# Kernel optimization log

Hardware: AMD Instinct MI355X
Metric: run time of the kernel (lower is better)

Reference implementation:

```python
import jax, jax.numpy as jnp
import numpy as np

HIDDEN = 512
FEAT = 128   # input features to GRU (inputs last dim = FEAT + 1 shock column)
BATCH = 128
SEQ = 512
DENSE1 = 64
BN_EPS = 1e-3  # Keras BatchNormalization default epsilon


def setup_inputs() -> dict:
    key = jax.random.key(0)
    ks = jax.random.split(key, 12)
    s = 0.05
    inputs = jax.random.normal(ks[0], (BATCH, SEQ, FEAT + 1), dtype=jnp.float32)
    return {
        "inputs": inputs,
        # GRU params (Keras reset_after=True layout: gates ordered z, r, h)
        "kernel": jax.random.normal(ks[1], (FEAT, 3 * HIDDEN), jnp.float32) * s,
        "recurrent_kernel": jax.random.normal(ks[2], (HIDDEN, 3 * HIDDEN), jnp.float32) * s,
        "bias": jax.random.normal(ks[3], (2, 3 * HIDDEN), jnp.float32) * s,  # [input_bias, recurrent_bias]
        # head
        "W1": jax.random.normal(ks[4], (HIDDEN, DENSE1), jnp.float32) * s,
        "b1": jnp.zeros((DENSE1,), jnp.float32),
        "gamma": jnp.ones((DENSE1,), jnp.float32),
        "beta": jnp.zeros((DENSE1,), jnp.float32),
        "moving_mean": jnp.zeros((DENSE1,), jnp.float32),
        "moving_var": jnp.ones((DENSE1,), jnp.float32),
        "W2": jax.random.normal(ks[5], (DENSE1, 1), jnp.float32) * s,
        "b2": jnp.zeros((1,), jnp.float32),
        "W_shock": jax.random.normal(ks[6], (1,), jnp.float32),
    }


def _gru_scan(x, h0, kernel, recurrent_kernel, bias):
    # x: [B,T,F] -> scan over time. Keras GRU v2 (reset_after=True):
    #   z = sig(x Wz + bzi + h Uz + bzr); r = sig(x Wr + ...);
    #   hh = tanh(x Wh + bhi + r*(h Uh + bhr)); h = z*h + (1-z)*hh
    b_i, b_r = bias[0], bias[1]
    xt = jnp.transpose(x, (1, 0, 2))  # [T,B,F]
    # precompute input projections for all steps: [T,B,3H]
    x_proj = jnp.einsum("tbf,fh->tbh", xt, kernel) + b_i
    H = h0.shape[-1]

    def step(h, xp):
        hp = h @ recurrent_kernel + b_r  # [B,3H]
        xz, xr, xh = xp[:, :H], xp[:, H:2 * H], xp[:, 2 * H:]
        hz, hr, hh_ = hp[:, :H], hp[:, H:2 * H], hp[:, 2 * H:]
        z = jax.nn.sigmoid(xz + hz)
        r = jax.nn.sigmoid(xr + hr)
        hh = jnp.tanh(xh + r * hh_)
        h_new = z * h + (1.0 - z) * hh
        return h_new, h_new

    state, seq = jax.lax.scan(step, h0, x_proj)
    return jnp.transpose(seq, (1, 0, 2)), state  # gru_out [B,T,H], state [B,H]


def reference(inputs, kernel, recurrent_kernel, bias, W1, b1, gamma, beta,
              moving_mean, moving_var, W2, b2, W_shock):
    x = inputs[:, :, :-1]            # [B,T,F]
    shock = inputs[:, :, -1]         # [B,T]
    h0 = jnp.zeros((x.shape[0], HIDDEN), x.dtype)
    gru_out, state = _gru_scan(x, h0, kernel, recurrent_kernel, bias)
    # shock effect: tile shock to [B,T,H], * W_shock, mean over time -> [B,H]
    shock_mean = jnp.mean(shock, axis=1, keepdims=True)  # [B,1]
    state = state + shock_mean * W_shock  # broadcasts to [B,H]
    # head (inference mode: dropout is identity, BN uses moving stats)
    h = jax.nn.relu(state @ W1 + b1)
    h = (h - moving_mean) * jax.lax.rsqrt(moving_var + BN_EPS) * gamma + beta
    return h @ W2 + b2  # [B,1]
```

## Files before the change

kernel.cpp:

```cpp
#include <hip/hip_runtime.h>
#include <hip/hip_fp16.h>

typedef _Float16 f16;
typedef _Float16 f16x8 __attribute__((ext_vector_type(8)));
typedef float    f32x4 __attribute__((ext_vector_type(4)));

#define HID 512
#define FEA 128
#define ROWSTR 129
#define SEQL 512
#define DEN1 64
#define NG 8
#define WPG 32
#define MB 16
#define GC 16
#define THREADS 256
#define KTOT 640

#define WS_CTR    0
#define WS_FLG    256
#define WS_HRING  4096
#define WS_SM     (WS_HRING + 262144)
#define WS_HPART  (WS_SM + 1024)
#define WS_END    (WS_HPART + 16384)

#define AT_LD(p)  __hip_atomic_load((p),  __ATOMIC_RELAXED, __HIP_MEMORY_SCOPE_AGENT)

union H4 { unsigned long long u; f16 h[4]; };

__device__ __forceinline__ f16x8 ld_h16(const f16* p) {
    f16x8 r;
    asm volatile("global_load_dwordx4 %0, %1, off sc0 sc1" : "=v"(r) : "v"(p));
    return r;
}
__device__ __forceinline__ void st_h64(void* p, unsigned long long v) {
    asm volatile("global_store_dwordx2 %0, %1, off sc0 sc1" :: "v"(p), "v"(v) : "memory");
}
__device__ __forceinline__ unsigned ld_flag(const unsigned* p) {
    unsigned r;
    asm volatile("global_load_dword %0, %1, off sc0 sc1" : "=v"(r) : "v"(p) : "memory");
    asm volatile("s_waitcnt vmcnt(0)" ::: "memory");
    return r;
}
__device__ __forceinline__ void st_flag(unsigned* p, unsigned v) {
    asm volatile("global_store_dword %0, %1, off sc0 sc1" :: "v"(p), "v"(v) : "memory");
}
__device__ __forceinline__ void wait_vm0() {
    asm volatile("s_waitcnt vmcnt(0)" ::: "memory");
    __builtin_amdgcn_sched_barrier(0);
}

__device__ __forceinline__ float sigmoid_f(float x) {
    x = fminf(fmaxf(x, -30.f), 30.f);
    return 1.f / (1.f + __expf(-x));
}
__device__ __forceinline__ float tanh_f(float x) {
    x = fminf(fmaxf(x, -15.f), 15.f);
    float e = __expf(2.f * x);
    return (e - 1.f) / (e + 1.f);
}

__global__ __launch_bounds__(THREADS)
void gru_fused(const float* __restrict__ inp, const float* __restrict__ Wk,
               const float* __restrict__ Rk,  const float* __restrict__ bias,
               const float* __restrict__ W1,  const float* __restrict__ b1,
               const float* __restrict__ gam, const float* __restrict__ bet,
               const float* __restrict__ mmn, const float* __restrict__ mvr,
               const float* __restrict__ W2,  const float* __restrict__ b2p,
               const float* __restrict__ Wsh, float* __restrict__ out,
               char* __restrict__ ws)
{
    __shared__ __align__(16) f16 Bl[KTOT * 48];
    __shared__ float red[4096];
    __shared__ __align__(8) f16 htile[256];

    const int tid  = threadIdx.x;
    const int g    = blockIdx.x & (NG - 1);
    const int wgk  = blockIdx.x >> 3;
    const int lane = tid & 63;
    const int wave = tid >> 6;
    const int j0   = wgk * GC;

    unsigned* ctr   = (unsigned*)(ws + WS_CTR);
    unsigned* flg   = (unsigned*)(ws + WS_FLG);
    f16*      hring = (f16*)(ws + WS_HRING);
    float*    smw   = (float*)(ws + WS_SM);
    float*    hpart = (float*)(ws + WS_HPART);

    for (int idx = tid; idx < KTOT * 48; idx += THREADS) {
        int kk  = idx / 48;
        int c   = idx - kk * 48;
        int col = (c >> 4) * HID + j0 + (c & 15);
        float v = (kk < HID) ? Rk[(size_t)kk * 1536 + col]
                             : Wk[(size_t)(kk - HID) * 1536 + col];
        Bl[((size_t)(kk >> 3) * 48 + c) * 8 + (kk & 7)] = (f16)v;
    }

    if (wgk < MB) {
        int b = g * MB + wgk;
        float a = 0.f;
        for (int t = tid; t < SEQL; t += THREADS)
            a += inp[((size_t)b * SEQL + t) * ROWSTR + FEA];
        red[tid] = a;
        __syncthreads();
        for (int s = THREADS / 2; s > 0; s >>= 1) {
            if (tid < s) red[tid] += red[tid + s];
            __syncthreads();
        }
        if (tid == 0) smw[b] = red[0] * (1.f / SEQL);
    }

    const int brow = tid >> 4;
    const int jcol = j0 + (tid & 15);
    const float bZ  = bias[jcol]           + bias[1536 + jcol];
    const float bR  = bias[512 + jcol]     + bias[1536 + 512 + jcol];
    const float bXH = bias[1024 + jcol];
    const float bHH = bias[1536 + 1024 + jcol];

    const int arow  = lane & 15;
    const int ahalf = lane >> 4;

    float xa[4][8];
    if (wave == 3) {
        const float* xb = inp + ((size_t)(g * MB + arow) * SEQL + 0) * ROWSTR + ahalf * 8;
        #pragma unroll
        for (int s = 0; s < 4; ++s)
            #pragma unroll
            for (int q = 0; q < 8; ++q)
                xa[s][q] = xb[s * 32 + q];
    }

    float hold = 0.f;
    __syncthreads();

    for (int t = 0; t < SEQL; ++t) {
        const int cur = t & 1;
        const f16* hb = hring + ((size_t)cur * NG + g) * MB * HID
                              + (size_t)arow * HID + ahalf * 8;

        f32x4 aZ = {0,0,0,0}, aR = {0,0,0,0}, aH = {0,0,0,0}, aX = {0,0,0,0};

        if (wave < 3) {
            f16x8 af[5];
            #pragma unroll
            for (int s = 0; s < 5; ++s)
                af[s] = ld_h16(hb + (wave * 5 + s) * 32);
            wait_vm0();
            #pragma unroll
            for (int s = 0; s < 5; ++s) {
                int ks = wave * 5 + s;
                const f16x8* bp = ((const f16x8*)Bl) + (ks * 4 + ahalf) * 48 + (lane & 15);
                f16x8 bz = bp[0], br = bp[16], bh = bp[32];
                aZ = __builtin_amdgcn_mfma_f32_16x16x32_f16(af[s], bz, aZ, 0, 0, 0);
                aR = __builtin_amdgcn_mfma_f32_16x16x32_f16(af[s], br, aR, 0, 0, 0);
                aH = __builtin_amdgcn_mfma_f32_16x16x32_f16(af[s], bh, aH, 0, 0, 0);
            }
        } else {
            f16x8 af0 = ld_h16(hb + 15 * 32);
            f16x8 afx[4];
            #pragma unroll
            for (int s = 0; s < 4; ++s) {
                f16x8 a;
                #pragma unroll
                for (int q = 0; q < 8; ++q) a[q] = (f16)xa[s][q];
                afx[s] = a;
            }
            wait_vm0();
            {
                const f16x8* bp = ((const f16x8*)Bl) + (15 * 4 + ahalf) * 48 + (lane & 15);
                aZ = __builtin_amdgcn_mfma_f32_16x16x32_f16(af0, bp[0],  aZ, 0, 0, 0);
                aR = __builtin_amdgcn_mfma_f32_16x16x32_f16(af0, bp[16], aR, 0, 0, 0);
                aH = __builtin_amdgcn_mfma_f32_16x16x32_f16(af0, bp[32], aH, 0, 0, 0);
            }
            #pragma unroll
            for (int s = 0; s < 4; ++s) {
                int ks = 16 + s;
                const f16x8* bp = ((const f16x8*)Bl) + (ks * 4 + ahalf) * 48 + (lane & 15);
                aZ = __builtin_amdgcn_mfma_f32_16x16x32_f16(afx[s], bp[0],  aZ, 0, 0, 0);
                aR = __builtin_amdgcn_mfma_f32_16x16x32_f16(afx[s], bp[16], aR, 0, 0, 0);
                aX = __builtin_amdgcn_mfma_f32_16x16x32_f16(afx[s], bp[32], aX, 0, 0, 0);
            }
        }

        #pragma unroll
        for (int i = 0; i < 4; ++i) {
            int ridx = (ahalf * 4 + i) * 16 + (lane & 15);
            red[wave * 1024 +       ridx] = aZ[i];
            red[wave * 1024 + 256 + ridx] = aR[i];
            red[wave * 1024 + 512 + ridx] = aH[i];
        }
        if (wave == 3) {
            #pragma unroll
            for (int i = 0; i < 4; ++i) {
                int ridx = (ahalf * 4 + i) * 16 + (lane & 15);
                red[3 * 1024 + 768 + ridx] = aX[i];
            }
            {
                int tt = (t + 1 < SEQL) ? t + 1 : SEQL - 1;
                const float* xb = inp + ((size_t)(g * MB + arow) * SEQL + tt) * ROWSTR + ahalf * 8;
                #pragma unroll
                for (int s = 0; s < 4; ++s)
                    #pragma unroll
                    for (int q = 0; q < 8; ++q)
                        xa[s][q] = xb[s * 32 + q];
            }
        }
        __syncthreads();

        float zp = red[tid] + red[1024 + tid] + red[2048 + tid] + red[3072 + tid];
        float rp = red[256 + tid] + red[1280 + tid] + red[2304 + tid] + red[3328 + tid];
        float hp = red[512 + tid] + red[1536 + tid] + red[2560 + tid] + red[3584 + tid];
        float xp = red[3840 + tid];

        float z = sigmoid_f(zp + bZ);
        float r = sigmoid_f(rp + bR);
        float hcand = tanh_f((xp + bXH) + r * (hp + bHH));
        float hnew = z * hold + (1.f - z) * hcand;
        f16 h16 = (f16)hnew;
        hold = (float)h16;
        htile[brow * 16 + (tid & 15)] = h16;
        __syncthreads();

        if (tid < 64) {
            int row = tid >> 2, q = tid & 3;
            unsigned long long val = *(const unsigned long long*)(htile + row * 16 + q * 4);
            st_h64(hring + (((size_t)(cur ^ 1) * NG + g) * MB + row) * HID + j0 + q * 4, val);
        }
        if (wave == 0) {
            asm volatile("s_waitcnt vmcnt(0)" ::: "memory");
            if (lane == 0) st_flag(flg + g * 32 + wgk, (unsigned)(t + 1));
            const unsigned want = (unsigned)(t + 1);
            for (;;) {
                unsigned v = ld_flag(flg + g * 32 + (lane & 31));
                if (__all((int)(v >= want))) break;
            }
        }
        __syncthreads();
    }

    const unsigned long long* hfq = (const unsigned long long*)
        (hring + ((size_t)g * MB + brow) * HID);
    const int sub = tid & 15;
    const int c0 = wgk * 2;
    float p0 = 0.f, p1 = 0.f, w0 = 0.f, w1 = 0.f;
    for (int c8 = 0; c8 < 8; ++c8) {
        H4 x; x.u = AT_LD(hfq + sub * 8 + c8);
        #pragma unroll
        for (int e = 0; e < 4; ++e) {
            int k = sub * 32 + c8 * 4 + e;
            float hv = (float)x.h[e];
            float a0 = W1[(size_t)k * DEN1 + c0];
            float a1 = W1[(size_t)k * DEN1 + c0 + 1];
            p0 += hv * a0; p1 += hv * a1; w0 += a0; w1 += a1;
        }
    }
    red[tid] = p0; red[256 + tid] = w0; red[512 + tid] = p1; red[768 + tid] = w1;
    __syncthreads();
    if (tid < 32) {
        int b = tid >> 1, cc = tid & 1;
        int c = c0 + cc;
        float dot = 0.f, wsum = 0.f;
        for (int i = 0; i < 16; ++i) {
            dot  += red[cc * 512 + b * 16 + i];
            wsum += red[cc * 512 + 256 + b * 16 + i];
        }
        float sW = smw[g * MB + b] * Wsh[0];
        float d = dot + sW * wsum + b1[c];
        d = fmaxf(d, 0.f);
        d = (d - mmn[c]) * rsqrtf(mvr[c] + 0.001f) * gam[c] + bet[c];
        red[1024 + tid] = d * W2[c];
    }
    __syncthreads();
    if (tid < MB)
        hpart[((size_t)g * WPG + wgk) * MB + tid] = red[1024 + tid * 2] + red[1024 + tid * 2 + 1];
    __syncthreads();
    if (tid == 0) {
        __builtin_amdgcn_fence(__ATOMIC_RELEASE, "agent");
        unsigned* c9 = ctr + g;
        unsigned old = __hip_atomic_fetch_add(c9, 1u, __ATOMIC_RELAXED, __HIP_MEMORY_SCOPE_AGENT);
        if (old != WPG - 1)
            while (__hip_atomic_load(c9, __ATOMIC_RELAXED, __HIP_MEMORY_SCOPE_AGENT) < WPG) {}
        __builtin_amdgcn_fence(__ATOMIC_ACQUIRE, "agent");
    }
    __syncthreads();
    if (wgk == 0 && tid < MB) {
        float o = b2p[0];
        for (int k = 0; k < WPG; ++k)
            o += hpart[((size_t)g * WPG + k) * MB + tid];
        out[g * MB + tid] = o;
    }
}

extern "C" void kernel_launch(void* const* d_in, const int* in_sizes, int n_in,
                              void* d_out, int out_size, void* d_ws, size_t ws_size,
                              hipStream_t stream) {
    (void)in_sizes; (void)n_in; (void)out_size; (void)ws_size;
    const float* inp  = (const float*)d_in[0];
    const float* Wk   = (const float*)d_in[1];
    const float* Rk   = (const float*)d_in[2];
    const float* bias = (const float*)d_in[3];
    const float* W1   = (const float*)d_in[4];
    const float* b1   = (const float*)d_in[5];
    const float* gam  = (const float*)d_in[6];
    const float* bet  = (const float*)d_in[7];
    const float* mmn  = (const float*)d_in[8];
    const float* mvr  = (const float*)d_in[9];
    const float* W2   = (const float*)d_in[10];
    const float* b2p  = (const float*)d_in[11];
    const float* Wsh  = (const float*)d_in[12];

    hipMemsetAsync(d_ws, 0, WS_END, stream);
    hipLaunchKernelGGL(gru_fused, dim3(NG * WPG), dim3(THREADS), 0, stream,
                       inp, Wk, Rk, bias, W1, b1, gam, bet, mmn, mvr, W2, b2p, Wsh,
                       (float*)d_out, (char*)d_ws);
}
```

Baseline: 1.386 ms.

## Split work by gate across waves and overlap input projection with flag wait

Each of waves 0-2 now computes one gate's full K=512 recurrent product instead of splitting K across four waves, which removes the cross-wave partial-sum reduction. Wave 3 computes the input projection for the next step, biases folded in and double-buffered in shared memory, while wave 0 spins on the inter-block flag barrier, taking it off the critical path. The h tile is written with per-thread 16-bit stores instead of an LDS staging pass, and custom barriers use only the needed waitcnt. The cost is 16 outstanding global loads per wave and many small stores, with a one-step-ahead x pipeline that must stay correctly synchronised.

```diff
diff --git a/kernel.cpp b/kernel.cpp
--- a/kernel.cpp
+++ b/kernel.cpp
@@ -15,7 +15,8 @@
 #define MB 16
 #define GC 16
 #define THREADS 256
-#define KTOT 640
+#define KH 512
+#define KX 128
 
 #define WS_CTR    0
 #define WS_FLG    256
@@ -24,30 +25,41 @@
 #define WS_HPART  (WS_SM + 1024)
 #define WS_END    (WS_HPART + 16384)
 
-#define AT_LD(p)  __hip_atomic_load((p),  __ATOMIC_RELAXED, __HIP_MEMORY_SCOPE_AGENT)
-
-union H4 { unsigned long long u; f16 h[4]; };
-
-__device__ __forceinline__ f16x8 ld_h16(const f16* p) {
-    f16x8 r;
-    asm volatile("global_load_dwordx4 %0, %1, off sc0 sc1" : "=v"(r) : "v"(p));
+__device__ __forceinline__ void st_h2(void* p, unsigned v) {
+    asm volatile("global_store_short %0, %1, off sc0 sc1" :: "v"(p), "v"(v) : "memory");
+}
+__device__ __forceinline__ unsigned long long ld_u64c(const void* p) {
+    unsigned long long r;
+    asm volatile("global_load_dwordx2 %0, %1, off sc0 sc1" : "=v"(r) : "v"(p));
+    asm volatile("s_waitcnt vmcnt(0)" ::: "memory");
     return r;
 }
-__device__ __forceinline__ void st_h64(void* p, unsigned long long v) {
-    asm volatile("global_store_dwordx2 %0, %1, off sc0 sc1" :: "v"(p), "v"(v) : "memory");
-}
-__device__ __forceinline__ unsigned ld_flag(const unsigned* p) {
+__device__ __forceinline__ unsigned ld_flag32(const unsigned* p) {
     unsigned r;
     asm volatile("global_load_dword %0, %1, off sc0 sc1" : "=v"(r) : "v"(p) : "memory");
     asm volatile("s_waitcnt vmcnt(0)" ::: "memory");
     return r;
 }
-__device__ __forceinline__ void st_flag(unsigned* p, unsigned v) {
+__device__ __forceinline__ void st_flag32(unsigned* p, unsigned v) {
     asm volatile("global_store_dword %0, %1, off sc0 sc1" :: "v"(p), "v"(v) : "memory");
 }
 __device__ __forceinline__ void wait_vm0() {
     asm volatile("s_waitcnt vmcnt(0)" ::: "memory");
     __builtin_amdgcn_sched_barrier(0);
+}
+__device__ __forceinline__ void barrier_lgkm() {
+    asm volatile("s_waitcnt lgkmcnt(0)" ::: "memory");
+    __builtin_amdgcn_sched_barrier(0);
+    __builtin_amdgcn_s_barrier();
+    __builtin_amdgcn_sched_barrier(0);
+    asm volatile("" ::: "memory");
+}
+__device__ __forceinline__ void barrier_vm0() {
+    asm volatile("s_waitcnt vmcnt(0) lgkmcnt(0)" ::: "memory");
+    __builtin_amdgcn_sched_barrier(0);
+    __builtin_amdgcn_s_barrier();
+    __builtin_amdgcn_sched_barrier(0);
+    asm volatile("" ::: "memory");
 }
 
 __device__ __forceinline__ float sigmoid_f(float x) {
@@ -70,9 +82,9 @@
                const float* __restrict__ Wsh, float* __restrict__ out,
                char* __restrict__ ws)
 {
-    __shared__ __align__(16) f16 Bl[KTOT * 48];
-    __shared__ float red[4096];
-    __shared__ __align__(8) f16 htile[256];
+    __shared__ __align__(16) f16 Bh[KH * 48];
+    __shared__ __align__(16) f16 Bx[KX * 48];
+    __shared__ float red[2304];
 
     const int tid  = threadIdx.x;
     const int g    = blockIdx.x & (NG - 1);
@@ -87,13 +99,15 @@
     float*    smw   = (float*)(ws + WS_SM);
     float*    hpart = (float*)(ws + WS_HPART);
 
-    for (int idx = tid; idx < KTOT * 48; idx += THREADS) {
-        int kk  = idx / 48;
-        int c   = idx - kk * 48;
+    for (int idx = tid; idx < KH * 48; idx += THREADS) {
+        int kk = idx / 48, c = idx - kk * 48;
         int col = (c >> 4) * HID + j0 + (c & 15);
-        float v = (kk < HID) ? Rk[(size_t)kk * 1536 + col]
-                             : Wk[(size_t)(kk - HID) * 1536 + col];
-        Bl[((size_t)(kk >> 3) * 48 + c) * 8 + (kk & 7)] = (f16)v;
+        Bh[((kk >> 3) * 48 + c) * 8 + (kk & 7)] = (f16)Rk[(size_t)kk * 1536 + col];
+    }
+    for (int idx = tid; idx < KX * 48; idx += THREADS) {
+        int kk = idx / 48, c = idx - kk * 48;
+        int col = (c >> 4) * HID + j0 + (c & 15);
+        Bx[((kk >> 3) * 48 + c) * 8 + (kk & 7)] = (f16)Wk[(size_t)kk * 1536 + col];
     }
 
     if (wgk < MB) {
@@ -112,139 +126,130 @@
 
     const int brow = tid >> 4;
     const int jcol = j0 + (tid & 15);
-    const float bZ  = bias[jcol]           + bias[1536 + jcol];
-    const float bR  = bias[512 + jcol]     + bias[1536 + 512 + jcol];
-    const float bXH = bias[1024 + jcol];
-    const float bHH = bias[1536 + 1024 + jcol];
-
     const int arow  = lane & 15;
     const int ahalf = lane >> 4;
+    const int lcol  = j0 + (lane & 15);
+    const float bZ3  = bias[lcol] + bias[1536 + lcol];
+    const float bR3  = bias[512 + lcol] + bias[1536 + 512 + lcol];
+    const float bX3  = bias[1024 + lcol];
+    const float bHH3 = bias[1536 + 1024 + lcol];
 
     float xa[4][8];
+
+    auto x_window = [&](int t) {
+        f16x8 afx[4];
+        #pragma unroll
+        for (int s = 0; s < 4; ++s) {
+            f16x8 a;
+            #pragma unroll
+            for (int q = 0; q < 8; ++q) a[q] = (f16)xa[s][q];
+            afx[s] = a;
+        }
+        f32x4 az = {0,0,0,0}, ar = {0,0,0,0}, ah = {0,0,0,0};
+        #pragma unroll
+        for (int s = 0; s < 4; ++s) {
+            const f16x8* bx = ((const f16x8*)Bx) + (s * 4 + ahalf) * 48 + (lane & 15);
+            az = __builtin_amdgcn_mfma_f32_16x16x32_f16(afx[s], bx[0],  az, 0, 0, 0);
+            ar = __builtin_amdgcn_mfma_f32_16x16x32_f16(afx[s], bx[16], ar, 0, 0, 0);
+            ah = __builtin_amdgcn_mfma_f32_16x16x32_f16(afx[s], bx[32], ah, 0, 0, 0);
+        }
+        float* xo = red + 768 + ((t + 1) & 1) * 768;
+        #pragma unroll
+        for (int i = 0; i < 4; ++i) {
+            int rix = (ahalf * 4 + i) * 16 + (lane & 15);
+            xo[rix]       = az[i] + bZ3;
+            xo[256 + rix] = ar[i] + bR3;
+            xo[512 + rix] = ah[i] + bX3;
+        }
+        int tt = (t + 2 < SEQL) ? t + 2 : SEQL - 1;
+        const float* xs = inp + ((size_t)(g * MB + arow) * SEQL + tt) * ROWSTR + ahalf * 8;
+        #pragma unroll
+        for (int s = 0; s < 4; ++s)
+            #pragma unroll
+            for (int q = 0; q < 8; ++q)
+                xa[s][q] = xs[s * 32 + q];
+    };
+
+    __syncthreads();
+
     if (wave == 3) {
-        const float* xb = inp + ((size_t)(g * MB + arow) * SEQL + 0) * ROWSTR + ahalf * 8;
+        const float* xs = inp + ((size_t)(g * MB + arow) * SEQL + 0) * ROWSTR + ahalf * 8;
         #pragma unroll
         for (int s = 0; s < 4; ++s)
             #pragma unroll
             for (int q = 0; q < 8; ++q)
-                xa[s][q] = xb[s * 32 + q];
+                xa[s][q] = xs[s * 32 + q];
+        x_window(-1);
     }
 
     float hold = 0.f;
-    __syncthreads();
 
     for (int t = 0; t < SEQL; ++t) {
         const int cur = t & 1;
-        const f16* hb = hring + ((size_t)cur * NG + g) * MB * HID
-                              + (size_t)arow * HID + ahalf * 8;
-
-        f32x4 aZ = {0,0,0,0}, aR = {0,0,0,0}, aH = {0,0,0,0}, aX = {0,0,0,0};
 
         if (wave < 3) {
-            f16x8 af[5];
-            #pragma unroll
-            for (int s = 0; s < 5; ++s)
-                af[s] = ld_h16(hb + (wave * 5 + s) * 32);
+            const f16* hb = hring + ((size_t)cur * NG + g) * MB * HID
+                                  + (size_t)arow * HID + ahalf * 8;
+            f16x8 af[16];
+            #pragma unroll
+            for (int s = 0; s < 16; ++s)
+                asm volatile("global_load_dwordx4 %0, %1, off offset:%c2 sc0 sc1"
+                             : "=v"(af[s]) : "v"(hb), "i"(s * 64));
             wait_vm0();
-            #pragma unroll
-            for (int s = 0; s < 5; ++s) {
-                int ks = wave * 5 + s;
-                const f16x8* bp = ((const f16x8*)Bl) + (ks * 4 + ahalf) * 48 + (lane & 15);
-                f16x8 bz = bp[0], br = bp[16], bh = bp[32];
-                aZ = __builtin_amdgcn_mfma_f32_16x16x32_f16(af[s], bz, aZ, 0, 0, 0);
-                aR = __builtin_amdgcn_mfma_f32_16x16x32_f16(af[s], br, aR, 0, 0, 0);
-                aH = __builtin_amdgcn_mfma_f32_16x16x32_f16(af[s], bh, aH, 0, 0, 0);
+            f32x4 a0 = {0,0,0,0}, a1 = {0,0,0,0};
+            const f16x8* bp = ((const f16x8*)Bh) + ahalf * 48 + wave * GC + (lane & 15);
+            #pragma unroll
+            for (int s = 0; s < 16; s += 2) {
+                a0 = __builtin_amdgcn_mfma_f32_16x16x32_f16(af[s],     bp[s * 192],       a0, 0, 0, 0);
+                a1 = __builtin_amdgcn_mfma_f32_16x16x32_f16(af[s + 1], bp[(s + 1) * 192], a1, 0, 0, 0);
             }
-        } else {
-            f16x8 af0 = ld_h16(hb + 15 * 32);
-            f16x8 afx[4];
-            #pragma unroll
-            for (int s = 0; s < 4; ++s) {
-                f16x8 a;
-                #pragma unroll
-                for (int q = 0; q < 8; ++q) a[q] = (f16)xa[s][q];
-                afx[s] = a;
-            }
-            wait_vm0();
-            {
-                const f16x8* bp = ((const f16x8*)Bl) + (15 * 4 + ahalf) * 48 + (lane & 15);
-                aZ = __builtin_amdgcn_mfma_f32_16x16x32_f16(af0, bp[0],  aZ, 0, 0, 0);
-                aR = __builtin_amdgcn_mfma_f32_16x16x32_f16(af0, bp[16], aR, 0, 0, 0);
-                aH = __builtin_amdgcn_mfma_f32_16x16x32_f16(af0, bp[32], aH, 0, 0, 0);
-            }
-            #pragma unroll
-            for (int s = 0; s < 4; ++s) {
-                int ks = 16 + s;
-                const f16x8* bp = ((const f16x8*)Bl) + (ks * 4 + ahalf) * 48 + (lane & 15);
-                aZ = __builtin_amdgcn_mfma_f32_16x16x32_f16(afx[s], bp[0],  aZ, 0, 0, 0);
-                aR = __builtin_amdgcn_mfma_f32_16x16x32_f16(afx[s], bp[16], aR, 0, 0, 0);
-                aX = __builtin_amdgcn_mfma_f32_16x16x32_f16(afx[s], bp[32], aX, 0, 0, 0);
-            }
-        }
-
-        #pragma unroll
-        for (int i = 0; i < 4; ++i) {
-            int ridx = (ahalf * 4 + i) * 16 + (lane & 15);
-            red[wave * 1024 +       ridx] = aZ[i];
-            red[wave * 1024 + 256 + ridx] = aR[i];
-            red[wave * 1024 + 512 + ridx] = aH[i];
-        }
-        if (wave == 3) {
-            #pragma unroll
-            for (int i = 0; i < 4; ++i) {
-                int ridx = (ahalf * 4 + i) * 16 + (lane & 15);
-                red[3 * 1024 + 768 + ridx] = aX[i];
-            }
-            {
-                int tt = (t + 1 < SEQL) ? t + 1 : SEQL - 1;
-                const float* xb = inp + ((size_t)(g * MB + arow) * SEQL + tt) * ROWSTR + ahalf * 8;
-                #pragma unroll
-                for (int s = 0; s < 4; ++s)
-                    #pragma unroll
-                    for (int q = 0; q < 8; ++q)
-                        xa[s][q] = xb[s * 32 + q];
-            }
-        }
-        __syncthreads();
-
-        float zp = red[tid] + red[1024 + tid] + red[2048 + tid] + red[3072 + tid];
-        float rp = red[256 + tid] + red[1280 + tid] + red[2304 + tid] + red[3328 + tid];
-        float hp = red[512 + tid] + red[1536 + tid] + red[2560 + tid] + red[3584 + tid];
-        float xp = red[3840 + tid];
-
-        float z = sigmoid_f(zp + bZ);
-        float r = sigmoid_f(rp + bR);
-        float hcand = tanh_f((xp + bXH) + r * (hp + bHH));
-        float hnew = z * hold + (1.f - z) * hcand;
-        f16 h16 = (f16)hnew;
-        hold = (float)h16;
-        htile[brow * 16 + (tid & 15)] = h16;
-        __syncthreads();
-
-        if (tid < 64) {
-            int row = tid >> 2, q = tid & 3;
-            unsigned long long val = *(const unsigned long long*)(htile + row * 16 + q * 4);
-            st_h64(hring + (((size_t)(cur ^ 1) * NG + g) * MB + row) * HID + j0 + q * 4, val);
-        }
+            f32x4 acc = a0 + a1;
+            float badd = (wave == 2) ? bHH3 : 0.f;
+            #pragma unroll
+            for (int i = 0; i < 4; ++i)
+                red[wave * 256 + (ahalf * 4 + i) * 16 + (lane & 15)] = acc[i] + badd;
+        }
+        barrier_lgkm();
+
+        {
+            float hzs = red[tid];
+            float hrs = red[256 + tid];
+            float hhs = red[512 + tid];
+            const float* xi = red + 768 + (t & 1) * 768;
+            float xzs = xi[tid], xrs = xi[256 + tid], xhs = xi[512 + tid];
+            float z = sigmoid_f(hzs + xzs);
+            float r = sigmoid_f(hrs + xrs);
+            float hc = tanh_f(xhs + r * hhs);
+            float hnew = z * hold + (1.f - z) * hc;
+            f16 h16 = (f16)hnew;
+            hold = (float)h16;
+            union { f16 h; unsigned short u; } cv; cv.h = h16;
+            st_h2(hring + (((size_t)(cur ^ 1) * NG + g) * MB + brow) * HID + jcol,
+                  (unsigned)cv.u);
+        }
+        barrier_vm0();
+
         if (wave == 0) {
-            asm volatile("s_waitcnt vmcnt(0)" ::: "memory");
-            if (lane == 0) st_flag(flg + g * 32 + wgk, (unsigned)(t + 1));
+            unsigned* fg = flg + g * 32;
+            if (lane == 0) st_flag32(fg + wgk, (unsigned)(t + 1));
             const unsigned want = (unsigned)(t + 1);
             for (;;) {
-                unsigned v = ld_flag(flg + g * 32 + (lane & 31));
+                unsigned v = ld_flag32(fg + (lane & 31));
                 if (__all((int)(v >= want))) break;
             }
-        }
-        __syncthreads();
-    }
-
-    const unsigned long long* hfq = (const unsigned long long*)
-        (hring + ((size_t)g * MB + brow) * HID);
+        } else if (wave == 3) {
+            x_window(t);
+        }
+        barrier_lgkm();
+    }
+
+    const f16* hf = hring + ((size_t)g * MB + brow) * HID;
     const int sub = tid & 15;
     const int c0 = wgk * 2;
     float p0 = 0.f, p1 = 0.f, w0 = 0.f, w1 = 0.f;
     for (int c8 = 0; c8 < 8; ++c8) {
-        H4 x; x.u = AT_LD(hfq + sub * 8 + c8);
+        union { unsigned long long u; f16 h[4]; } x;
+        x.u = ld_u64c(hf + sub * 32 + c8 * 4);
         #pragma unroll
         for (int e = 0; e < 4; ++e) {
             int k = sub * 32 + c8 * 4 + e;
@@ -254,6 +259,7 @@
             p0 += hv * a0; p1 += hv * a1; w0 += a0; w1 += a1;
         }
     }
+    __syncthreads();
     red[tid] = p0; red[256 + tid] = w0; red[512 + tid] = p1; red[768 + tid] = w1;
     __syncthreads();
     if (tid < 32) {
```

After: 1.751 ms. +26.4%, slower.
